# Performance work log

Hardware: AMD Instinct MI355X
Metric: run time of the kernel (lower is better)

Reference implementation:

```python
import jax, jax.numpy as jnp
import numpy as np

ID, IH, IW = 8, 16, 16
HEADS, DIM_HEAD = 8, 32
INP, OUP = 256, 256
B = 4
N = ID * IH * IW  # 2048
INNER = HEADS * DIM_HEAD  # 256
SCALE = DIM_HEAD ** -0.5


def _make_relative_pos():
    # Faithful to the torch ctor: 3D coords, pairwise diffs, linearize, shift to >=0
    z, y, x = np.meshgrid(np.arange(ID), np.arange(IH), np.arange(IW), indexing='ij')
    coords = np.stack([z.ravel(), y.ravel(), x.ravel()], axis=1)  # [N,3]
    rel = coords[:, None, :] - coords[None, :, :]                 # [N,N,3]
    rp = rel[:, :, 0] * (IH * IW) + rel[:, :, 1] * IW + rel[:, :, 2]
    rp = rp - rp.min()
    return jnp.asarray(rp, dtype=jnp.int32)                       # [N,N]


def setup_inputs() -> dict:
    key = jax.random.key(0)
    k1, k2, k3, k4, k5 = jax.random.split(key, 5)
    table_size = ID * IH * IW * 8  # 16384, as in nn.Embedding ctor
    return {
        "x": jax.random.normal(k1, (B, N, INP), dtype=jnp.float32),
        "w_qkv": jax.random.normal(k2, (INP, 3 * INNER), dtype=jnp.float32) * (INP ** -0.5),
        "bias_table": jax.random.normal(k3, (table_size, 1), dtype=jnp.float32),
        "w_out": jax.random.normal(k4, (INNER, OUP), dtype=jnp.float32) * (INNER ** -0.5),
        "b_out": jax.random.normal(k5, (OUP,), dtype=jnp.float32),
        "relative_pos": _make_relative_pos(),
    }


def reference(x, w_qkv, bias_table, w_out, b_out, relative_pos):
    Bb, Nn, C = x.shape
    qkv = x @ w_qkv                                   # [B, N, 3*H*D]
    qkv = qkv.reshape(Bb, Nn, 3, HEADS, DIM_HEAD)
    qkv = jnp.transpose(qkv, (2, 0, 3, 1, 4))         # [3, B, H, N, D]
    q, k, v = qkv[0], qkv[1], qkv[2]
    q = q * SCALE
    attn = jnp.einsum('bhnd,bhmd->bhnm', q, k)        # [B, H, N, N]
    bias = bias_table[relative_pos, 0]                # [N, N], shared across B,H
    attn = attn + bias
    attn = jax.nn.softmax(attn, axis=-1)
    out = jnp.einsum('bhnm,bhmd->bhnd', attn, v)      # [B, H, N, D]
    out = jnp.transpose(out, (0, 2, 1, 3)).reshape(Bb, Nn, INNER)
    return out @ w_out + b_out                        # dropout p=0 -> identity
```

## Files before the change

### kernel.cpp

```cpp
#include <hip/hip_runtime.h>

typedef unsigned short u16;
typedef unsigned int u32;
typedef __attribute__((ext_vector_type(8))) short bf16x8;
typedef __attribute__((ext_vector_type(4))) short bf16x4;
typedef __attribute__((ext_vector_type(4))) float f32x4;

#define MFMA16(a, b, c) __builtin_amdgcn_mfma_f32_16x16x32_bf16(a, b, c, 0, 0, 0)
#define MFMAK16(a, b, c) __builtin_amdgcn_mfma_f32_16x16x16bf16_1k(a, b, c, 0, 0, 0)

__device__ __forceinline__ float hw_exp2(float x) { return __builtin_amdgcn_exp2f(x); }

__device__ __forceinline__ u16 f2bf(float f) {
    union { float f; u32 i; } v; v.f = f;
    u32 x = v.i;
    return (u16)((x + 0x7FFFu + ((x >> 16) & 1u)) >> 16);
}

__device__ __forceinline__ u32 cvt_pk_bf16(float lo, float hi) {
    u32 r;
    asm("v_cvt_pk_bf16_f32 %0, %1, %2" : "=v"(r) : "v"(lo), "v"(hi));
    return r;
}

__device__ __forceinline__ bf16x8 pack8(float4 a, float4 b) {
    union { u32 u[4]; bf16x8 v; } r;
    r.u[0] = cvt_pk_bf16(a.x, a.y);
    r.u[1] = cvt_pk_bf16(a.z, a.w);
    r.u[2] = cvt_pk_bf16(b.x, b.y);
    r.u[3] = cvt_pk_bf16(b.z, b.w);
    return r.v;
}

__global__ __launch_bounds__(256) void k_gemm_qkv(const float* __restrict__ x,
                                                  const float* __restrict__ wqkv,
                                                  u16* __restrict__ qkv) {
    __shared__ __align__(16) u16 smem[16896];
    const int tid = threadIdx.x;
    const int wave = tid >> 6, lane = tid & 63, quad = lane >> 4, ql = lane & 15;
    const int by = blockIdx.y;
    const int mbase = blockIdx.x * 128 + (wave & 1) * 64;
    const float QSCALE2 = 0.2550566756538019f;

    {
        const int c4 = (tid & 15) * 4;
        const float sc = (by < 4) ? QSCALE2 : 1.0f;
        for (int kk = tid >> 4; kk < 256; kk += 16) {
            float4 w4 = *(const float4*)(wqkv + (size_t)kk * 768 + by * 64 + c4);
            smem[(c4 + 0) * 264 + kk] = f2bf(w4.x * sc);
            smem[(c4 + 1) * 264 + kk] = f2bf(w4.y * sc);
            smem[(c4 + 2) * 264 + kk] = f2bf(w4.z * sc);
            smem[(c4 + 3) * 264 + kk] = f2bf(w4.w * sc);
        }
    }
    __syncthreads();

    const int nrow = (wave >> 1) * 32;
    f32x4 acc[4][2];
#pragma unroll
    for (int i = 0; i < 4; ++i)
#pragma unroll
        for (int j = 0; j < 2; ++j) acc[i][j] = (f32x4){0.f, 0.f, 0.f, 0.f};
#pragma unroll
    for (int ks = 0; ks < 8; ++ks) {
        bf16x8 af[4], bfm[2];
#pragma unroll
        for (int ms = 0; ms < 4; ++ms) {
            const float* ap = x + (size_t)(mbase + ms * 16 + ql) * 256 + ks * 32 + quad * 8;
            af[ms] = pack8(*(const float4*)ap, *(const float4*)(ap + 4));
        }
#pragma unroll
        for (int ns = 0; ns < 2; ++ns)
            bfm[ns] = *(const bf16x8*)&smem[(nrow + ns * 16 + ql) * 264 + ks * 32 + quad * 8];
#pragma unroll
        for (int ms = 0; ms < 4; ++ms)
#pragma unroll
            for (int ns = 0; ns < 2; ++ns)
                acc[ms][ns] = MFMA16(af[ms], bfm[ns], acc[ms][ns]);
    }
    __syncthreads();

    u16* slds = smem;
    const int t = (by * 64) >> 8;
    if (t < 2) {
        const int rowb = (wave & 1) * 64, colb = (wave >> 1) * 32;
#pragma unroll
        for (int ms = 0; ms < 4; ++ms)
#pragma unroll
            for (int ns = 0; ns < 2; ++ns)
#pragma unroll
                for (int r = 0; r < 4; ++r)
                    slds[(rowb + ms * 16 + quad * 4 + r) * 68 + colb + ns * 16 + ql] =
                        f2bf(acc[ms][ns][r]);
        __syncthreads();
        u16* base = qkv + (size_t)t * 2097152;
#pragma unroll
        for (int p = 0; p < 8; ++p) {
            int c = p * 256 + tid;
            int row = c >> 4, ch = c & 15;
            uint2 w = *(const uint2*)&slds[row * 68 + ch * 4];
            int n = blockIdx.x * 128 + row;
            int col = by * 64 + ch * 4;
            int h = (col & 255) >> 5, d = col & 31;
            *(uint2*)(base + ((size_t)((n >> 11) * 8 + h) * 2048 + (n & 2047)) * 32 + d) = w;
        }
    } else {
        const int hl = wave >> 1, nb = (wave & 1) * 64;
#pragma unroll
        for (int ms = 0; ms < 4; ++ms)
#pragma unroll
            for (int ns = 0; ns < 2; ++ns) {
                uint2 pp;
                pp.x = cvt_pk_bf16(acc[ms][ns][0], acc[ms][ns][1]);
                pp.y = cvt_pk_bf16(acc[ms][ns][2], acc[ms][ns][3]);
                *(uint2*)&slds[(hl * 32 + ns * 16 + ql) * 136 + nb + ms * 16 + quad * 4] = pp;
            }
        __syncthreads();
        u16* vbase = qkv + (size_t)2 * 2097152;
#pragma unroll
        for (int p = 0; p < 4; ++p) {
            int c = p * 256 + tid;
            int row = c >> 4, ch = c & 15;
            bf16x8 w = *(const bf16x8*)&slds[row * 136 + ch * 8];
            int n0 = blockIdx.x * 128 + ch * 8;
            int h = (by & 3) * 2 + (row >> 5), d = row & 31;
            *(bf16x8*)(vbase + (size_t)((n0 >> 11) * 8 + h) * 65536 +
                       (size_t)d * 2048 + (n0 & 2047)) = w;
        }
    }
}

__global__ __launch_bounds__(256, 2) void k_attn(const u16* __restrict__ q,
                                                 const u16* __restrict__ k,
                                                 const u16* __restrict__ vT,
                                                 const float* __restrict__ table,
                                                 u16* __restrict__ att) {
    __shared__ __align__(16) u16 kbuf[2][2][2048];
    __shared__ __align__(16) u16 vbuf[2][2][2048];
    __shared__ float tbl2[2176];
    const int tid = threadIdx.x;
    const int bh = blockIdx.x & 31, qt = blockIdx.x >> 5;
    const int wave = tid >> 6, lane = tid & 63, quad = lane >> 4, ql = lane & 15;
    const float LOG2E = 1.4426950408889634f;

    const u16* kbh = k + (size_t)bh * 65536;
    const u16* vbh = vT + (size_t)bh * 65536;

    const int krow = wave * 16 + (lane >> 2);
    const u16* kg = kbh + krow * 32 + ((((lane & 3) ^ ((lane >> 3) & 3))) << 3);
    const int vd = wave * 8 + (lane >> 3);
    const u16* vg = vbh + (size_t)vd * 2048 + (((lane & 7) ^ (vd & 7)) << 3);

#define GLDS(SRC, DST) __builtin_amdgcn_global_load_lds(                         \
        (const __attribute__((address_space(1))) void*)(SRC),                    \
        (__attribute__((address_space(3))) void*)(DST), 16, 0, 0)
#define DMA(BUF, PAIR) do {                                                      \
    GLDS(kg + (PAIR) * 4096,        &kbuf[BUF][0][wave * 512]);                  \
    GLDS(kg + (PAIR) * 4096 + 2048, &kbuf[BUF][1][wave * 512]);                  \
    GLDS(vg + (PAIR) * 128,         &vbuf[BUF][0][wave * 512]);                  \
    GLDS(vg + (PAIR) * 128 + 64,    &vbuf[BUF][1][wave * 512]);                  \
} while (0)

    DMA(0, 0);

    const float4* tg = (const float4*)(table + qt * 128);
    for (int i = tid; i < 544; i += 256) {
        float4 t = tg[i];
        t.x *= LOG2E; t.y *= LOG2E; t.z *= LOG2E; t.w *= LOG2E;
        ((float4*)tbl2)[i] = t;
    }

    const int qr0 = qt * 128 + wave * 32 + ql;
    bf16x8 qf[2];
    qf[0] = *(const bf16x8*)(q + ((size_t)bh * 2048 + qr0) * 32 + quad * 8);
    qf[1] = *(const bf16x8*)(q + ((size_t)bh * 2048 + qr0 + 16) * 32 + quad * 8);
    const int bloc0 = wave * 32 + ql + 2047 - quad * 4;
    const int kro = ((quad ^ ((ql >> 1) & 3)) << 3);

    bf16x4 ones4;
#pragma unroll
    for (int i = 0; i < 4; ++i) ones4[i] = (short)0x3F80;

    f32x4 oT0[2], oT1[2], oL[2];
#pragma unroll
    for (int qh = 0; qh < 2; ++qh) {
        oT0[qh] = (f32x4){0.f, 0.f, 0.f, 0.f};
        oT1[qh] = (f32x4){0.f, 0.f, 0.f, 0.f};
        oL[qh]  = (f32x4){0.f, 0.f, 0.f, 0.f};
    }

    __syncthreads();

    for (int pr = 0; pr < 16; ++pr) {
        const int buf = pr & 1;

        f32x4 bc[2][5];
#pragma unroll
        for (int t = 0; t < 2; ++t) {
            const int bkt = bloc0 - (pr * 2 + t) * 64;
#pragma unroll
            for (int g = 0; g < 5; ++g) {
                const int b0 = bkt + 16 * g - 51;
                bc[t][g] = (f32x4){tbl2[b0 + 3], tbl2[b0 + 2], tbl2[b0 + 1], tbl2[b0 + 0]};
            }
        }
        __builtin_amdgcn_sched_barrier(0);

        if (pr < 15) DMA(buf ^ 1, pr + 1);

#pragma unroll
        for (int t = 0; t < 2; ++t) {
            const u16* kb = &kbuf[buf][t][0];
            const u16* vb = &vbuf[buf][t][0];
            bf16x8 kf[4];
            bf16x4 va[2][4];
#pragma unroll
            for (int j = 0; j < 4; ++j)
                kf[j] = *(const bf16x8*)(kb + (j * 16 + ql) * 32 + kro);
#pragma unroll
            for (int dt = 0; dt < 2; ++dt)
#pragma unroll
                for (int j = 0; j < 4; ++j) {
                    int nloc = j * 16 + quad * 4;
                    int slot = (nloc >> 3) ^ (ql & 7);
                    va[dt][j] = *(const bf16x4*)(vb + (dt * 16 + ql) * 64 +
                                                 slot * 8 + (nloc & 7));
                }

#pragma unroll
            for (int qh = 0; qh < 2; ++qh) {
                __builtin_amdgcn_s_setprio(1);
                f32x4 s[4];
#pragma unroll
                for (int j = 0; j < 4; ++j)
                    s[j] = MFMA16(kf[j], qf[qh], bc[t][qh + 3 - j]);
#pragma unroll
                for (int j = 0; j < 4; ++j)
#pragma unroll
                    for (int r = 0; r < 4; ++r)
                        s[j][r] = hw_exp2(s[j][r]);
#pragma unroll
                for (int j = 0; j < 4; ++j) {
                    union { u32 u[2]; bf16x4 v; } pj;
                    pj.u[0] = __builtin_amdgcn_perm(__float_as_uint(s[j][1]),
                                                    __float_as_uint(s[j][0]), 0x07060302u);
                    pj.u[1] = __builtin_amdgcn_perm(__float_as_uint(s[j][3]),
                                                    __float_as_uint(s[j][2]), 0x07060302u);
                    oT0[qh] = MFMAK16(va[0][j], pj.v, oT0[qh]);
                    oT1[qh] = MFMAK16(va[1][j], pj.v, oT1[qh]);
                    oL[qh]  = MFMAK16(ones4, pj.v, oL[qh]);
                }
                __builtin_amdgcn_s_setprio(0);
            }
        }
        __syncthreads();
    }
#undef DMA
#undef GLDS

#pragma unroll
    for (int qh = 0; qh < 2; ++qh) {
        float inv = 1.0f / oL[qh][0];
        size_t base = ((size_t)bh * 2048 + qr0 + qh * 16) * 32;
#pragma unroll
        for (int dt = 0; dt < 2; ++dt) {
            const f32x4& o = dt ? oT1[qh] : oT0[qh];
            uint2 pp;
            pp.x = cvt_pk_bf16(o[0] * inv, o[1] * inv);
            pp.y = cvt_pk_bf16(o[2] * inv, o[3] * inv);
            *(uint2*)(att + base + dt * 16 + quad * 4) = pp;
        }
    }
}

__global__ __launch_bounds__(256) void k_gemm_out(const u16* __restrict__ attq,
                                                  const float* __restrict__ wout,
                                                  const float* __restrict__ bout,
                                                  float* __restrict__ out) {
    __shared__ __align__(16) u16 bs[16896];
    const int tid = threadIdx.x;
    const int wave = tid >> 6, lane = tid & 63, quad = lane >> 4, ql = lane & 15;
    const int by = blockIdx.y;
    const int mbase = blockIdx.x * 128 + (wave & 1) * 64;

    {
        const int c4 = (tid & 15) * 4;
        for (int kk = tid >> 4; kk < 256; kk += 16) {
            float4 w4 = *(const float4*)(wout + (size_t)kk * 256 + by * 64 + c4);
            bs[(c4 + 0) * 264 + kk] = f2bf(w4.x);
            bs[(c4 + 1) * 264 + kk] = f2bf(w4.y);
            bs[(c4 + 2) * 264 + kk] = f2bf(w4.z);
            bs[(c4 + 3) * 264 + kk] = f2bf(w4.w);
        }
    }
    __syncthreads();

    const int nrow = (wave >> 1) * 32;
    f32x4 acc[4][2];
#pragma unroll
    for (int i = 0; i < 4; ++i)
#pragma unroll
        for (int j = 0; j < 2; ++j) acc[i][j] = (f32x4){0.f, 0.f, 0.f, 0.f};
#pragma unroll
    for (int ks = 0; ks < 8; ++ks) {
        bf16x8 af[4], bfm[2];
#pragma unroll
        for (int ms = 0; ms < 4; ++ms) {
            int row = mbase + ms * 16 + ql;
            af[ms] = *(const bf16x8*)(attq +
                ((size_t)((row >> 11) * 8 + ks) * 2048 + (row & 2047)) * 32 + quad * 8);
        }
#pragma unroll
        for (int ns = 0; ns < 2; ++ns)
            bfm[ns] = *(const bf16x8*)&bs[(nrow + ns * 16 + ql) * 264 + ks * 32 + quad * 8];
#pragma unroll
        for (int ms = 0; ms < 4; ++ms)
#pragma unroll
            for (int ns = 0; ns < 2; ++ns)
                acc[ms][ns] = MFMA16(af[ms], bfm[ns], acc[ms][ns]);
    }
#pragma unroll
    for (int ms = 0; ms < 4; ++ms)
#pragma unroll
        for (int ns = 0; ns < 2; ++ns)
#pragma unroll
            for (int r = 0; r < 4; ++r) {
                int Mrow = mbase + ms * 16 + quad * 4 + r;
                int col = by * 64 + (wave >> 1) * 32 + ns * 16 + ql;
                out[(size_t)Mrow * 256 + col] = acc[ms][ns][r] + bout[col];
            }
}

extern "C" void kernel_launch(void* const* d_in, const int* in_sizes, int n_in,
                              void* d_out, int out_size, void* d_ws, size_t ws_size,
                              hipStream_t stream) {
    const float* x    = (const float*)d_in[0];
    const float* wqkv = (const float*)d_in[1];
    const float* btab = (const float*)d_in[2];
    const float* wout = (const float*)d_in[3];
    const float* bout = (const float*)d_in[4];
    float* out = (float*)d_out;

    if (ws_size < (size_t)12582912) return;
    u16* qkv = (u16*)d_ws;

    hipLaunchKernelGGL(k_gemm_qkv, dim3(64, 12), dim3(256), 0, stream, x, wqkv, qkv);
    hipLaunchKernelGGL(k_attn, dim3(512), dim3(256), 0, stream,
                       qkv, qkv + 2097152, qkv + 2 * 2097152, btab, qkv);
    hipLaunchKernelGGL(k_gemm_out, dim3(64, 4), dim3(256), 0, stream, qkv, wout, bout, out);
}
```

Measured before the change: 144.3 us.

## Precompute reversed, shifted bias-table copies and read bias via float4 global loads

Adds an extra row of blocks to the QKV GEMM launch. These blocks write four reversed copies of the bias table, each pre-scaled by log2(e) and shifted by 0..3 elements, into workspace. The attention kernel drops its per-block LDS staging of the table and loads each 4-wide bias group directly from global memory as an aligned float4. This removes the LDS footprint and the scalar LDS reads, which could help occupancy. In exchange it adds global or L2 traffic inside the main loop and needs more workspace.

```diff
diff --git a/kernel.cpp b/kernel.cpp
--- a/kernel.cpp
+++ b/kernel.cpp
@@ -34,11 +34,24 @@
 
 __global__ __launch_bounds__(256) void k_gemm_qkv(const float* __restrict__ x,
                                                   const float* __restrict__ wqkv,
+                                                  const float* __restrict__ btab,
+                                                  float* __restrict__ R4,
                                                   u16* __restrict__ qkv) {
     __shared__ __align__(16) u16 smem[16896];
     const int tid = threadIdx.x;
+    const int by = blockIdx.y;
+
+    if (by == 12) {
+        const float LOG2E = 1.4426950408889634f;
+        const int j = blockIdx.x * 256 + tid;
+#pragma unroll
+        for (int a = 0; a < 4; ++a)
+            if (j + a <= 16383)
+                R4[(size_t)a * 16384 + j] = LOG2E * btab[16383 - j - a];
+        return;
+    }
+
     const int wave = tid >> 6, lane = tid & 63, quad = lane >> 4, ql = lane & 15;
-    const int by = blockIdx.y;
     const int mbase = blockIdx.x * 128 + (wave & 1) * 64;
     const float QSCALE2 = 0.2550566756538019f;
 
@@ -133,15 +146,13 @@
 __global__ __launch_bounds__(256, 2) void k_attn(const u16* __restrict__ q,
                                                  const u16* __restrict__ k,
                                                  const u16* __restrict__ vT,
-                                                 const float* __restrict__ table,
+                                                 const float* __restrict__ R4,
                                                  u16* __restrict__ att) {
     __shared__ __align__(16) u16 kbuf[2][2][2048];
     __shared__ __align__(16) u16 vbuf[2][2][2048];
-    __shared__ float tbl2[2176];
     const int tid = threadIdx.x;
     const int bh = blockIdx.x & 31, qt = blockIdx.x >> 5;
     const int wave = tid >> 6, lane = tid & 63, quad = lane >> 4, ql = lane & 15;
-    const float LOG2E = 1.4426950408889634f;
 
     const u16* kbh = k + (size_t)bh * 65536;
     const u16* vbh = vT + (size_t)bh * 65536;
@@ -163,13 +174,6 @@
 
     DMA(0, 0);
 
-    const float4* tg = (const float4*)(table + qt * 128);
-    for (int i = tid; i < 544; i += 256) {
-        float4 t = tg[i];
-        t.x *= LOG2E; t.y *= LOG2E; t.z *= LOG2E; t.w *= LOG2E;
-        ((float4*)tbl2)[i] = t;
-    }
-
     const int qr0 = qt * 128 + wave * 32 + ql;
     bf16x8 qf[2];
     qf[0] = *(const bf16x8*)(q + ((size_t)bh * 2048 + qr0) * 32 + quad * 8);
@@ -177,6 +181,9 @@
     const int bloc0 = wave * 32 + ql + 2047 - quad * 4;
     const int kro = ((quad ^ ((ql >> 1) & 3)) << 3);
 
+    const int ubase = 16431 - qt * 128 - bloc0;
+    const float* Rpl = R4 + (size_t)(ubase & 3) * 16384 + (ubase - (ubase & 3));
+
     bf16x4 ones4;
 #pragma unroll
     for (int i = 0; i < 4; ++i) ones4[i] = (short)0x3F80;
@@ -197,11 +204,11 @@
         f32x4 bc[2][5];
 #pragma unroll
         for (int t = 0; t < 2; ++t) {
-            const int bkt = bloc0 - (pr * 2 + t) * 64;
+            const int kt = pr * 2 + t;
 #pragma unroll
             for (int g = 0; g < 5; ++g) {
-                const int b0 = bkt + 16 * g - 51;
-                bc[t][g] = (f32x4){tbl2[b0 + 3], tbl2[b0 + 2], tbl2[b0 + 1], tbl2[b0 + 0]};
+                float4 v = *(const float4*)(Rpl + 64 * kt - 16 * g);
+                bc[t][g] = (f32x4){v.x, v.y, v.z, v.w};
             }
         }
         __builtin_amdgcn_sched_barrier(0);
@@ -341,11 +348,12 @@
     const float* bout = (const float*)d_in[4];
     float* out = (float*)d_out;
 
-    if (ws_size < (size_t)12582912) return;
+    if (ws_size < (size_t)12845056) return;
     u16* qkv = (u16*)d_ws;
-
-    hipLaunchKernelGGL(k_gemm_qkv, dim3(64, 12), dim3(256), 0, stream, x, wqkv, qkv);
+    float* R4 = (float*)(qkv + 6291456);
+
+    hipLaunchKernelGGL(k_gemm_qkv, dim3(64, 13), dim3(256), 0, stream, x, wqkv, btab, R4, qkv);
     hipLaunchKernelGGL(k_attn, dim3(512), dim3(256), 0, stream,
-                       qkv, qkv + 2097152, qkv + 2 * 2097152, btab, qkv);
+                       qkv, qkv + 2097152, qkv + 2 * 2097152, R4, qkv);
     hipLaunchKernelGGL(k_gemm_out, dim3(64, 4), dim3(256), 0, stream, qkv, wout, bout, out);
 }
```

Result: slower. 147.9 us (+2.5%).

## Split attention over two KV halves and merge partials in output GEMM

Applied to the files above, without the earlier changes.

The attention kernel now splits the key/value sequence into two halves, launching twice as many blocks. Each block writes unnormalized fp32 partial outputs and row sums to a new workspace instead of a normalized bf16 result. The output projection GEMM combines the two partials and normalizes them while loading its A operand. This is meant to raise parallelism and occupancy for the attention stage (512 blocks to 1024, launch bounds raised to 4). The cost is extra fp32 traffic for the partials and more work in the output GEMM's loads. Merging without a max shift is valid here because the kernel does not subtract a running max.

```diff
diff --git a/kernel.cpp b/kernel.cpp
--- a/kernel.cpp
+++ b/kernel.cpp
@@ -30,6 +30,16 @@
     r.u[2] = cvt_pk_bf16(b.x, b.y);
     r.u[3] = cvt_pk_bf16(b.z, b.w);
     return r.v;
+}
+
+__device__ __forceinline__ bf16x8 comb8(const float* p0, const float* p1, float inv) {
+    float4 a0 = *(const float4*)p0, a1 = *(const float4*)(p0 + 4);
+    float4 c0 = *(const float4*)p1, c1 = *(const float4*)(p1 + 4);
+    float4 lo = {(a0.x + c0.x) * inv, (a0.y + c0.y) * inv,
+                 (a0.z + c0.z) * inv, (a0.w + c0.w) * inv};
+    float4 hi = {(a1.x + c1.x) * inv, (a1.y + c1.y) * inv,
+                 (a1.z + c1.z) * inv, (a1.w + c1.w) * inv};
+    return pack8(lo, hi);
 }
 
 __global__ __launch_bounds__(256) void k_gemm_qkv(const float* __restrict__ x,
@@ -130,16 +140,17 @@
     }
 }
 
-__global__ __launch_bounds__(256, 2) void k_attn(const u16* __restrict__ q,
+__global__ __launch_bounds__(256, 4) void k_attn(const u16* __restrict__ q,
                                                  const u16* __restrict__ k,
                                                  const u16* __restrict__ vT,
                                                  const float* __restrict__ table,
-                                                 u16* __restrict__ att) {
+                                                 float* __restrict__ po,
+                                                 float* __restrict__ lbuf) {
     __shared__ __align__(16) u16 kbuf[2][2][2048];
     __shared__ __align__(16) u16 vbuf[2][2][2048];
-    __shared__ float tbl2[2176];
+    __shared__ float tbl2[1152];
     const int tid = threadIdx.x;
-    const int bh = blockIdx.x & 31, qt = blockIdx.x >> 5;
+    const int bh = blockIdx.x & 31, qt = (blockIdx.x >> 5) & 15, kvh = blockIdx.x >> 9;
     const int wave = tid >> 6, lane = tid & 63, quad = lane >> 4, ql = lane & 15;
     const float LOG2E = 1.4426950408889634f;
 
@@ -161,10 +172,11 @@
     GLDS(vg + (PAIR) * 128 + 64,    &vbuf[BUF][1][wave * 512]);                  \
 } while (0)
 
-    DMA(0, 0);
-
-    const float4* tg = (const float4*)(table + qt * 128);
-    for (int i = tid; i < 544; i += 256) {
+    const int gp0 = kvh * 8;
+    DMA(0, gp0);
+
+    const float4* tg = (const float4*)(table + (1024 + qt * 128 - kvh * 1024));
+    for (int i = tid; i < 288; i += 256) {
         float4 t = tg[i];
         t.x *= LOG2E; t.y *= LOG2E; t.z *= LOG2E; t.w *= LOG2E;
         ((float4*)tbl2)[i] = t;
@@ -174,7 +186,7 @@
     bf16x8 qf[2];
     qf[0] = *(const bf16x8*)(q + ((size_t)bh * 2048 + qr0) * 32 + quad * 8);
     qf[1] = *(const bf16x8*)(q + ((size_t)bh * 2048 + qr0 + 16) * 32 + quad * 8);
-    const int bloc0 = wave * 32 + ql + 2047 - quad * 4;
+    const int bloc0 = wave * 32 + ql + 1023 - quad * 4;
     const int kro = ((quad ^ ((ql >> 1) & 3)) << 3);
 
     bf16x4 ones4;
@@ -191,7 +203,7 @@
 
     __syncthreads();
 
-    for (int pr = 0; pr < 16; ++pr) {
+    for (int pr = 0; pr < 8; ++pr) {
         const int buf = pr & 1;
 
         f32x4 bc[2][5];
@@ -206,7 +218,7 @@
         }
         __builtin_amdgcn_sched_barrier(0);
 
-        if (pr < 15) DMA(buf ^ 1, pr + 1);
+        if (pr < 7) DMA(buf ^ 1, gp0 + pr + 1);
 
 #pragma unroll
         for (int t = 0; t < 2; ++t) {
@@ -260,20 +272,19 @@
 
 #pragma unroll
     for (int qh = 0; qh < 2; ++qh) {
-        float inv = 1.0f / oL[qh][0];
-        size_t base = ((size_t)bh * 2048 + qr0 + qh * 16) * 32;
+        size_t rbase = ((size_t)(kvh * 32 + bh) * 2048 + qr0 + qh * 16) * 32;
 #pragma unroll
         for (int dt = 0; dt < 2; ++dt) {
             const f32x4& o = dt ? oT1[qh] : oT0[qh];
-            uint2 pp;
-            pp.x = cvt_pk_bf16(o[0] * inv, o[1] * inv);
-            pp.y = cvt_pk_bf16(o[2] * inv, o[3] * inv);
-            *(uint2*)(att + base + dt * 16 + quad * 4) = pp;
-        }
-    }
-}
-
-__global__ __launch_bounds__(256) void k_gemm_out(const u16* __restrict__ attq,
+            *(float4*)(po + rbase + dt * 16 + quad * 4) = (float4){o[0], o[1], o[2], o[3]};
+        }
+        if (quad == 0)
+            lbuf[(size_t)(kvh * 32 + bh) * 2048 + qr0 + qh * 16] = oL[qh][0];
+    }
+}
+
+__global__ __launch_bounds__(256) void k_gemm_out(const float* __restrict__ po,
+                                                  const float* __restrict__ lb,
                                                   const float* __restrict__ wout,
                                                   const float* __restrict__ bout,
                                                   float* __restrict__ out) {
@@ -306,9 +317,11 @@
         bf16x8 af[4], bfm[2];
 #pragma unroll
         for (int ms = 0; ms < 4; ++ms) {
-            int row = mbase + ms * 16 + ql;
-            af[ms] = *(const bf16x8*)(attq +
-                ((size_t)((row >> 11) * 8 + ks) * 2048 + (row & 2047)) * 32 + quad * 8);
+            int n = mbase + ms * 16 + ql;
+            size_t bhp = (size_t)((n >> 11) * 8 + ks);
+            const float* p0 = po + (bhp * 2048 + (n & 2047)) * 32 + quad * 8;
+            float ls = lb[bhp * 2048 + (n & 2047)] + lb[65536 + bhp * 2048 + (n & 2047)];
+            af[ms] = comb8(p0, p0 + 2097152, 1.0f / ls);
         }
 #pragma unroll
         for (int ns = 0; ns < 2; ++ns)
@@ -341,11 +354,13 @@
     const float* bout = (const float*)d_in[4];
     float* out = (float*)d_out;
 
-    if (ws_size < (size_t)12582912) return;
+    if (ws_size < (size_t)29884416) return;
     u16* qkv = (u16*)d_ws;
+    float* po = (float*)(qkv + 6291456);
+    float* lb = po + 2 * 2097152;
 
     hipLaunchKernelGGL(k_gemm_qkv, dim3(64, 12), dim3(256), 0, stream, x, wqkv, qkv);
-    hipLaunchKernelGGL(k_attn, dim3(512), dim3(256), 0, stream,
-                       qkv, qkv + 2097152, qkv + 2 * 2097152, btab, qkv);
-    hipLaunchKernelGGL(k_gemm_out, dim3(64, 4), dim3(256), 0, stream, qkv, wout, bout, out);
-}
+    hipLaunchKernelGGL(k_attn, dim3(1024), dim3(256), 0, stream,
+                       qkv, qkv + 2097152, qkv + 2 * 2097152, btab, po, lb);
+    hipLaunchKernelGGL(k_gemm_out, dim3(64, 4), dim3(256), 0, stream, po, lb, wout, bout, out);
+}
```

Measured after the change: 173.1 us. 1.2x slower.
